# Kernel tuning notes

Measured on AMD Instinct MI355X. Metric: run time of the kernel, lower is better.

The kernel has to match this reference:

```python
import jax, jax.numpy as jnp
import numpy as np


def setup_inputs() -> dict:
    key = jax.random.key(0)
    bs, width, length = 4, 1536, 2048  # width = 3 * num_heads * ch = 3*8*64
    qkv = jax.random.normal(key, (bs, width, length), dtype=jnp.float32)
    return {"qkv": qkv, "num_heads": 8}


def reference(qkv, num_heads):
    bs, width, length = qkv.shape
    assert width % (3 * num_heads) == 0
    ch = width // (3 * num_heads)
    q, k, v = jnp.split(qkv, 3, axis=1)  # each [bs, num_heads*ch, length]
    scale = 1.0 / np.sqrt(np.sqrt(ch))  # applied to both q and k (total 1/sqrt(ch))
    q = (q * scale).reshape(bs * num_heads, ch, length)
    k = (k * scale).reshape(bs * num_heads, ch, length)
    v = v.reshape(bs * num_heads, ch, length)
    # weight[b, t, s] = sum_c q[b,c,t] * k[b,c,s]
    weight = jnp.einsum('bct,bcs->bts', q, k)
    weight = jax.nn.softmax(weight.astype(jnp.float32), axis=-1).astype(weight.dtype)
    # a[b, c, t] = sum_s weight[b,t,s] * v[b,c,s]
    a = jnp.einsum('bts,bcs->bct', weight, v)
    return a.reshape(bs, num_heads * ch, length)
```

## Files before the change

kernel.cpp:

```cpp
#include <hip/hip_runtime.h>

typedef float f32x16 __attribute__((ext_vector_type(16)));
typedef float f32x2 __attribute__((ext_vector_type(2)));
typedef short short8 __attribute__((ext_vector_type(8)));
typedef unsigned short u16;
typedef unsigned int u32;

#define SEQ_L 2048

#if __has_builtin(__builtin_amdgcn_exp2f)
#define EXP2(x) __builtin_amdgcn_exp2f(x)
#else
#define EXP2(x) exp2f(x)
#endif

__device__ __forceinline__ u32 pk2bf(float lo, float hi) {
#if __has_builtin(__builtin_amdgcn_cvt_pk_bf16_f32)
    typedef __bf16 bf16x2_t __attribute__((ext_vector_type(2)));
    union { bf16x2_t v; u32 i; } w;
    w.v = __builtin_amdgcn_cvt_pk_bf16_f32(lo, hi);
    return w.i;
#else
    union { float f; u32 i; } a, b; a.f = lo; b.f = hi;
    return ((a.i + 0x8000u) >> 16) | ((b.i + 0x8000u) & 0xFFFF0000u);
#endif
}

#define KT_U16 (64 * 64)
#define VT_STRIDE 72
#define VT_U16 (64 * VT_STRIDE)
#define GRP_U16 (KT_U16 + VT_U16)
#define SMEM_U16 33792

__global__ __launch_bounds__(512, 2)
void attn_kernel(const float* __restrict__ qkv, float* __restrict__ out) {
    const int tid  = threadIdx.x;
    const int lane = tid & 63;
    const int wv   = tid >> 6;
    const int g    = wv >> 2;
    const int wvin = wv & 3;
    const int col  = lane & 31;
    const int half = lane >> 5;

    const int gid  = blockIdx.x;
    const int head = gid & 31;
    const int tb   = gid >> 5;
    const int t0   = tb * 256 + wvin * 64;
    const int bb   = head >> 3, hh = head & 7;

    const size_t qoff = ((size_t)bb * 1536 + (size_t)hh * 64) * SEQ_L;
    const float* qp = qkv + qoff;
    const float* kp = qp + (size_t)512  * SEQ_L;
    const float* vp = qp + (size_t)1024 * SEQ_L;
    float* op = out + ((size_t)bb * 512 + (size_t)hh * 64) * SEQ_L;

    __shared__ __align__(16) u16 smem[SMEM_U16];
    u16* ktg = smem + g * GRP_U16;
    u16* vtg = ktg + KT_U16;

    const int gtid = tid & 255;
    const int sgrp = gtid & 15;
    const int rq   = gtid >> 4;
    const int sbase0 = g * 1024;

    u16* kw[4];
#pragma unroll
    for (int j = 0; j < 4; ++j) {
        int s = 4 * sgrp + j;
        int sw = ((s >> 2) ^ s) & 7;
        kw[j] = ktg + s * 64 + (((rq >> 1) ^ sw) << 3) + ((rq & 1) << 2);
    }
    const int vcoloff = ((sgrp >> 2) << 4) + ((sgrp & 1) << 3) + (((sgrp >> 1) & 1) << 2);
    u16* vw = vtg + rq * VT_STRIDE + vcoloff;

    const int sw_r = ((col >> 2) ^ col) & 7;
    int kco[4];
#pragma unroll
    for (int ks = 0; ks < 4; ++ks) kco[ks] = ((2 * ks + half) ^ sw_r) << 3;
    const u16* krb0 = ktg + col * 64;
    const u16* krb1 = ktg + (32 + col) * 64;
    const u16* vrb0 = vtg + col * VT_STRIDE + half * 8;
    const u16* vrb1 = vtg + (32 + col) * VT_STRIDE + half * 8;

    const int tA = t0 + col;
    const int tB = tA + 32;
    const float qscale = 0.18033688f;
    short8 qfA[4], qfB[4];
#pragma unroll
    for (int ks = 0; ks < 4; ++ks) {
        union { u32 u[4]; short8 v; } qa, qb;
#pragma unroll
        for (int e2 = 0; e2 < 4; ++e2) {
            int c = ks * 16 + half * 8 + 2 * e2;
            const float* c0 = qp + (size_t)c * SEQ_L;
            const float* c1 = qp + (size_t)(c + 1) * SEQ_L;
            qa.u[e2] = pk2bf(c0[tA] * qscale, c1[tA] * qscale);
            qb.u[e2] = pk2bf(c0[tB] * qscale, c1[tB] * qscale);
        }
        qfA[ks] = qa.v; qfB[ks] = qb.v;
    }

    f32x16 zacc;
#pragma unroll
    for (int r = 0; r < 16; ++r) zacc[r] = 0.0f;

    f32x16 accO[2][2];
#pragma unroll
    for (int tt = 0; tt < 2; ++tt)
#pragma unroll
        for (int m = 0; m < 2; ++m)
#pragma unroll
            for (int r = 0; r < 16; ++r) accO[tt][m][r] = 0.0f;
    f32x2 lsA = {0.0f, 0.0f}, lsB = {0.0f, 0.0f};

    float4 kreg[4], vreg[4];
#pragma unroll
    for (int rr = 0; rr < 4; ++rr) {
        kreg[rr] = *(const float4*)(kp + (size_t)(4 * rq + rr) * SEQ_L + sbase0 + 4 * sgrp);
        vreg[rr] = *(const float4*)(vp + (size_t)(rq + 16 * rr) * SEQ_L + sbase0 + 4 * sgrp);
    }

    for (int it = 0; it < 16; ++it) {
        __syncthreads();
#pragma unroll
        for (int j = 0; j < 4; ++j) {
            uint2 w;
            w.x = pk2bf(kreg[0][j], kreg[1][j]);
            w.y = pk2bf(kreg[2][j], kreg[3][j]);
            *(uint2*)kw[j] = w;
        }
#pragma unroll
        for (int rr = 0; rr < 4; ++rr) {
            uint2 w;
            w.x = pk2bf(vreg[rr].x, vreg[rr].y);
            w.y = pk2bf(vreg[rr].z, vreg[rr].w);
            *(uint2*)(vw + 16 * rr * VT_STRIDE) = w;
        }
        __syncthreads();

        if (it + 1 < 16) {
            const int sn = sbase0 + (it + 1) * 64;
#pragma unroll
            for (int rr = 0; rr < 4; ++rr) {
                kreg[rr] = *(const float4*)(kp + (size_t)(4 * rq + rr) * SEQ_L + sn + 4 * sgrp);
                vreg[rr] = *(const float4*)(vp + (size_t)(rq + 16 * rr) * SEQ_L + sn + 4 * sgrp);
            }
        }

        f32x16 accA[2], accB[2];
#pragma unroll
        for (int mb = 0; mb < 2; ++mb) {
            const u16* rb = mb ? krb1 : krb0;
            short8 kf0 = *(const short8*)(rb + kco[0]);
            accA[mb] = __builtin_amdgcn_mfma_f32_32x32x16_bf16(kf0, qfA[0], zacc, 0, 0, 0);
            accB[mb] = __builtin_amdgcn_mfma_f32_32x32x16_bf16(kf0, qfB[0], zacc, 0, 0, 0);
#pragma unroll
            for (int ks = 1; ks < 4; ++ks) {
                short8 kf = *(const short8*)(rb + kco[ks]);
                accA[mb] = __builtin_amdgcn_mfma_f32_32x32x16_bf16(kf, qfA[ks], accA[mb], 0, 0, 0);
                accB[mb] = __builtin_amdgcn_mfma_f32_32x32x16_bf16(kf, qfB[ks], accB[mb], 0, 0, 0);
            }
        }

        u32 pregA[2][8], pregB[2][8];
#pragma unroll
        for (int mb = 0; mb < 2; ++mb) {
            f32x2 a2[4], b2[4];
#pragma unroll
            for (int u2 = 0; u2 < 8; ++u2) {
                float ax = EXP2(accA[mb][2 * u2]);
                float ay = EXP2(accA[mb][2 * u2 + 1]);
                pregA[mb][u2] = pk2bf(ax, ay);
                f32x2 av = {ax, ay};
                if (u2 < 4) a2[u2] = av; else a2[u2 - 4] += av;
            }
            lsA += (a2[0] + a2[1]) + (a2[2] + a2[3]);
#pragma unroll
            for (int u2 = 0; u2 < 8; ++u2) {
                float bx = EXP2(accB[mb][2 * u2]);
                float by = EXP2(accB[mb][2 * u2 + 1]);
                pregB[mb][u2] = pk2bf(bx, by);
                f32x2 bv = {bx, by};
                if (u2 < 4) b2[u2] = bv; else b2[u2 - 4] += bv;
            }
            lsB += (b2[0] + b2[1]) + (b2[2] + b2[3]);
        }

#pragma unroll
        for (int mk = 0; mk < 4; ++mk) {
            int mb = mk >> 1, kb = mk & 1;
            union { u32 u[4]; short8 v; } bfA, bfB;
#pragma unroll
            for (int i = 0; i < 4; ++i) {
                bfA.u[i] = pregA[mb][4 * kb + i];
                bfB.u[i] = pregB[mb][4 * kb + i];
            }
#pragma unroll
            for (int mbc = 0; mbc < 2; ++mbc) {
                short8 vf = *(const short8*)((mbc ? vrb1 : vrb0) + mk * 16);
                accO[0][mbc] = __builtin_amdgcn_mfma_f32_32x32x16_bf16(vf, bfA.v, accO[0][mbc], 0, 0, 0);
                accO[1][mbc] = __builtin_amdgcn_mfma_f32_32x32x16_bf16(vf, bfB.v, accO[1][mbc], 0, 0, 0);
            }
        }
    }

    float lsum[2];
    lsum[0] = lsA[0] + lsA[1];
    lsum[1] = lsB[0] + lsB[1];

    __syncthreads();
    float* ep = (float*)smem;
    if (g == 1) {
#pragma unroll
        for (int tt = 0; tt < 2; ++tt) {
            float* row = ep + ((wvin * 64 + lane) * 2 + tt) * 33;
#pragma unroll
            for (int mbc = 0; mbc < 2; ++mbc)
#pragma unroll
                for (int r = 0; r < 16; ++r) row[mbc * 16 + r] = accO[tt][mbc][r];
            row[32] = lsum[tt];
        }
    }
    __syncthreads();
    if (g == 0) {
#pragma unroll
        for (int tt = 0; tt < 2; ++tt) {
            const float* row = ep + ((wvin * 64 + lane) * 2 + tt) * 33;
#pragma unroll
            for (int mbc = 0; mbc < 2; ++mbc)
#pragma unroll
                for (int r = 0; r < 16; ++r) accO[tt][mbc][r] += row[mbc * 16 + r];
            float lt = lsum[tt] + row[32];
            float ltot = lt + __shfl_xor(lt, 32, 64);
            float inv = 1.0f / ltot;
            const int t = tt ? tB : tA;
#pragma unroll
            for (int mbc = 0; mbc < 2; ++mbc) {
#pragma unroll
                for (int r = 0; r < 16; ++r) {
                    int c = mbc * 32 + (r & 3) + 8 * (r >> 2) + 4 * half;
                    op[(size_t)c * SEQ_L + t] = accO[tt][mbc][r] * inv;
                }
            }
        }
    }
}

extern "C" void kernel_launch(void* const* d_in, const int* in_sizes, int n_in,
                              void* d_out, int out_size, void* d_ws, size_t ws_size,
                              hipStream_t stream) {
    (void)in_sizes; (void)n_in; (void)d_ws; (void)ws_size; (void)out_size;
    const float* qkv = (const float*)d_in[0];
    float* out = (float*)d_out;
    attn_kernel<<<dim3(256), dim3(512), 0, stream>>>(qkv, out);
}
```

Baseline: 118.8 us.

## Process 128-key tiles per iteration to halve barriers and loop trips

Doubles the key/value tile staged in shared memory per loop iteration from 64 to 128 keys, splitting the compute into two 64-key sub-blocks. This halves the number of __syncthreads pairs and global-load/publish phases, giving more MFMA work between barriers. It doubles the prefetch register buffers, which raises VGPR pressure under the two-blocks-per-CU launch bound and risks spilling.

```diff
diff --git a/kernel.cpp b/kernel.cpp
--- a/kernel.cpp
+++ b/kernel.cpp
@@ -26,11 +26,11 @@
 #endif
 }
 
-#define KT_U16 (64 * 64)
-#define VT_STRIDE 72
+#define KT_U16 (128 * 64)
+#define VT_STRIDE 136
 #define VT_U16 (64 * VT_STRIDE)
 #define GRP_U16 (KT_U16 + VT_U16)
-#define SMEM_U16 33792
+#define SMEM_U16 (2 * GRP_U16)
 
 __global__ __launch_bounds__(512, 2)
 void attn_kernel(const float* __restrict__ qkv, float* __restrict__ out) {
@@ -77,8 +77,12 @@
     int kco[4];
 #pragma unroll
     for (int ks = 0; ks < 4; ++ks) kco[ks] = ((2 * ks + half) ^ sw_r) << 3;
-    const u16* krb0 = ktg + col * 64;
-    const u16* krb1 = ktg + (32 + col) * 64;
+    const u16* krb[2][2];
+#pragma unroll
+    for (int sub = 0; sub < 2; ++sub) {
+        krb[sub][0] = ktg + (sub * 64 + col) * 64;
+        krb[sub][1] = ktg + (sub * 64 + 32 + col) * 64;
+    }
     const u16* vrb0 = vtg + col * VT_STRIDE + half * 8;
     const u16* vrb1 = vtg + (32 + col) * VT_STRIDE + half * 8;
 
@@ -113,93 +117,102 @@
             for (int r = 0; r < 16; ++r) accO[tt][m][r] = 0.0f;
     f32x2 lsA = {0.0f, 0.0f}, lsB = {0.0f, 0.0f};
 
-    float4 kreg[4], vreg[4];
-#pragma unroll
-    for (int rr = 0; rr < 4; ++rr) {
-        kreg[rr] = *(const float4*)(kp + (size_t)(4 * rq + rr) * SEQ_L + sbase0 + 4 * sgrp);
-        vreg[rr] = *(const float4*)(vp + (size_t)(rq + 16 * rr) * SEQ_L + sbase0 + 4 * sgrp);
-    }
-
-    for (int it = 0; it < 16; ++it) {
+    float4 kreg[8], vreg[8];
+    auto load_tile = [&](int sb) {
+#pragma unroll
+        for (int rr = 0; rr < 4; ++rr) {
+            const float* kr = kp + (size_t)(4 * rq + rr) * SEQ_L + sb + 4 * sgrp;
+            const float* vr = vp + (size_t)(rq + 16 * rr) * SEQ_L + sb + 4 * sgrp;
+            kreg[rr]     = *(const float4*)(kr);
+            kreg[4 + rr] = *(const float4*)(kr + 64);
+            vreg[rr]     = *(const float4*)(vr);
+            vreg[4 + rr] = *(const float4*)(vr + 64);
+        }
+    };
+    auto publish = [&]() {
+#pragma unroll
+        for (int hs = 0; hs < 2; ++hs) {
+#pragma unroll
+            for (int j = 0; j < 4; ++j) {
+                uint2 w;
+                w.x = pk2bf(kreg[4 * hs + 0][j], kreg[4 * hs + 1][j]);
+                w.y = pk2bf(kreg[4 * hs + 2][j], kreg[4 * hs + 3][j]);
+                *(uint2*)(kw[j] + hs * 64 * 64) = w;
+            }
+#pragma unroll
+            for (int rr = 0; rr < 4; ++rr) {
+                uint2 w;
+                w.x = pk2bf(vreg[4 * hs + rr].x, vreg[4 * hs + rr].y);
+                w.y = pk2bf(vreg[4 * hs + rr].z, vreg[4 * hs + rr].w);
+                *(uint2*)(vw + 16 * rr * VT_STRIDE + hs * 64) = w;
+            }
+        }
+    };
+
+    load_tile(sbase0);
+
+    for (int it = 0; it < 8; ++it) {
         __syncthreads();
-#pragma unroll
-        for (int j = 0; j < 4; ++j) {
-            uint2 w;
-            w.x = pk2bf(kreg[0][j], kreg[1][j]);
-            w.y = pk2bf(kreg[2][j], kreg[3][j]);
-            *(uint2*)kw[j] = w;
-        }
-#pragma unroll
-        for (int rr = 0; rr < 4; ++rr) {
-            uint2 w;
-            w.x = pk2bf(vreg[rr].x, vreg[rr].y);
-            w.y = pk2bf(vreg[rr].z, vreg[rr].w);
-            *(uint2*)(vw + 16 * rr * VT_STRIDE) = w;
-        }
+        publish();
         __syncthreads();
-
-        if (it + 1 < 16) {
-            const int sn = sbase0 + (it + 1) * 64;
-#pragma unroll
-            for (int rr = 0; rr < 4; ++rr) {
-                kreg[rr] = *(const float4*)(kp + (size_t)(4 * rq + rr) * SEQ_L + sn + 4 * sgrp);
-                vreg[rr] = *(const float4*)(vp + (size_t)(rq + 16 * rr) * SEQ_L + sn + 4 * sgrp);
-            }
-        }
-
-        f32x16 accA[2], accB[2];
-#pragma unroll
-        for (int mb = 0; mb < 2; ++mb) {
-            const u16* rb = mb ? krb1 : krb0;
-            short8 kf0 = *(const short8*)(rb + kco[0]);
-            accA[mb] = __builtin_amdgcn_mfma_f32_32x32x16_bf16(kf0, qfA[0], zacc, 0, 0, 0);
-            accB[mb] = __builtin_amdgcn_mfma_f32_32x32x16_bf16(kf0, qfB[0], zacc, 0, 0, 0);
-#pragma unroll
-            for (int ks = 1; ks < 4; ++ks) {
-                short8 kf = *(const short8*)(rb + kco[ks]);
-                accA[mb] = __builtin_amdgcn_mfma_f32_32x32x16_bf16(kf, qfA[ks], accA[mb], 0, 0, 0);
-                accB[mb] = __builtin_amdgcn_mfma_f32_32x32x16_bf16(kf, qfB[ks], accB[mb], 0, 0, 0);
-            }
-        }
-
-        u32 pregA[2][8], pregB[2][8];
-#pragma unroll
-        for (int mb = 0; mb < 2; ++mb) {
-            f32x2 a2[4], b2[4];
-#pragma unroll
-            for (int u2 = 0; u2 < 8; ++u2) {
-                float ax = EXP2(accA[mb][2 * u2]);
-                float ay = EXP2(accA[mb][2 * u2 + 1]);
-                pregA[mb][u2] = pk2bf(ax, ay);
-                f32x2 av = {ax, ay};
-                if (u2 < 4) a2[u2] = av; else a2[u2 - 4] += av;
-            }
-            lsA += (a2[0] + a2[1]) + (a2[2] + a2[3]);
-#pragma unroll
-            for (int u2 = 0; u2 < 8; ++u2) {
-                float bx = EXP2(accB[mb][2 * u2]);
-                float by = EXP2(accB[mb][2 * u2 + 1]);
-                pregB[mb][u2] = pk2bf(bx, by);
-                f32x2 bv = {bx, by};
-                if (u2 < 4) b2[u2] = bv; else b2[u2 - 4] += bv;
-            }
-            lsB += (b2[0] + b2[1]) + (b2[2] + b2[3]);
-        }
-
-#pragma unroll
-        for (int mk = 0; mk < 4; ++mk) {
-            int mb = mk >> 1, kb = mk & 1;
-            union { u32 u[4]; short8 v; } bfA, bfB;
-#pragma unroll
-            for (int i = 0; i < 4; ++i) {
-                bfA.u[i] = pregA[mb][4 * kb + i];
-                bfB.u[i] = pregB[mb][4 * kb + i];
-            }
-#pragma unroll
-            for (int mbc = 0; mbc < 2; ++mbc) {
-                short8 vf = *(const short8*)((mbc ? vrb1 : vrb0) + mk * 16);
-                accO[0][mbc] = __builtin_amdgcn_mfma_f32_32x32x16_bf16(vf, bfA.v, accO[0][mbc], 0, 0, 0);
-                accO[1][mbc] = __builtin_amdgcn_mfma_f32_32x32x16_bf16(vf, bfB.v, accO[1][mbc], 0, 0, 0);
+        if (it + 1 < 8) load_tile(sbase0 + (it + 1) * 128);
+
+#pragma unroll
+        for (int sub = 0; sub < 2; ++sub) {
+            f32x16 accA[2], accB[2];
+#pragma unroll
+            for (int mb = 0; mb < 2; ++mb) {
+                const u16* rb = krb[sub][mb];
+                short8 kf0 = *(const short8*)(rb + kco[0]);
+                accA[mb] = __builtin_amdgcn_mfma_f32_32x32x16_bf16(kf0, qfA[0], zacc, 0, 0, 0);
+                accB[mb] = __builtin_amdgcn_mfma_f32_32x32x16_bf16(kf0, qfB[0], zacc, 0, 0, 0);
+#pragma unroll
+                for (int ks = 1; ks < 4; ++ks) {
+                    short8 kf = *(const short8*)(rb + kco[ks]);
+                    accA[mb] = __builtin_amdgcn_mfma_f32_32x32x16_bf16(kf, qfA[ks], accA[mb], 0, 0, 0);
+                    accB[mb] = __builtin_amdgcn_mfma_f32_32x32x16_bf16(kf, qfB[ks], accB[mb], 0, 0, 0);
+                }
+            }
+
+            u32 pregA[2][8], pregB[2][8];
+#pragma unroll
+            for (int mb = 0; mb < 2; ++mb) {
+                f32x2 a2[4], b2[4];
+#pragma unroll
+                for (int u2 = 0; u2 < 8; ++u2) {
+                    float ax = EXP2(accA[mb][2 * u2]);
+                    float ay = EXP2(accA[mb][2 * u2 + 1]);
+                    pregA[mb][u2] = pk2bf(ax, ay);
+                    f32x2 av = {ax, ay};
+                    if (u2 < 4) a2[u2] = av; else a2[u2 - 4] += av;
+                }
+                lsA += (a2[0] + a2[1]) + (a2[2] + a2[3]);
+#pragma unroll
+                for (int u2 = 0; u2 < 8; ++u2) {
+                    float bx = EXP2(accB[mb][2 * u2]);
+                    float by = EXP2(accB[mb][2 * u2 + 1]);
+                    pregB[mb][u2] = pk2bf(bx, by);
+                    f32x2 bv = {bx, by};
+                    if (u2 < 4) b2[u2] = bv; else b2[u2 - 4] += bv;
+                }
+                lsB += (b2[0] + b2[1]) + (b2[2] + b2[3]);
+            }
+
+#pragma unroll
+            for (int mk = 0; mk < 4; ++mk) {
+                int mb = mk >> 1, kb = mk & 1;
+                union { u32 u[4]; short8 v; } bfA, bfB;
+#pragma unroll
+                for (int i = 0; i < 4; ++i) {
+                    bfA.u[i] = pregA[mb][4 * kb + i];
+                    bfB.u[i] = pregB[mb][4 * kb + i];
+                }
+#pragma unroll
+                for (int mbc = 0; mbc < 2; ++mbc) {
+                    short8 vf = *(const short8*)((mbc ? vrb1 : vrb0) + sub * 64 + mk * 16);
+                    accO[0][mbc] = __builtin_amdgcn_mfma_f32_32x32x16_bf16(vf, bfA.v, accO[0][mbc], 0, 0, 0);
+                    accO[1][mbc] = __builtin_amdgcn_mfma_f32_32x32x16_bf16(vf, bfB.v, accO[1][mbc], 0, 0, 0);
+                }
             }
         }
     }
```

Result: slower. 143.0 us (+20.4%).
